# Kernel tuning notes

Measured on AMD Instinct MI355X. Metric: run time of the kernel, lower is better.

## Reference

```python
import jax, jax.numpy as jnp
import numpy as np

B, S, HID = 2, 2048, 2048
H, D = 16, 128  # heads, head_dim == kernel_hidden_size
GATE_NORM = 16.0
CLAMP_MIN = -50.0


def gla(q, k, v, gk):
    # fused_recurrent_gla: S_t = diag(exp(gk_t)) S_{t-1} + k_t^T v_t; o_t = (q_t*scale) @ S_t
    # q,k,v,gk: [B,H,S,D]
    scale = D ** -0.5
    qs = jnp.moveaxis(q, 2, 0) * scale  # [S,B,H,D]
    ks = jnp.moveaxis(k, 2, 0)
    vs = jnp.moveaxis(v, 2, 0)
    gs = jnp.moveaxis(gk, 2, 0)

    def step(state, xs):
        q_t, k_t, v_t, g_t = xs  # each [B,H,D]
        state = state * jnp.exp(g_t)[..., None] + k_t[..., None] * v_t[..., None, :]
        o_t = jnp.einsum('bhk,bhkv->bhv', q_t, state)
        return state, o_t

    init = jnp.zeros((q.shape[0], H, D, D), q.dtype)
    _, out = jax.lax.scan(step, init, (qs, ks, vs, gs))
    return jnp.moveaxis(out, 0, 2)  # [B,H,S,D]


def setup_inputs() -> dict:
    key = jax.random.key(0)
    ks = jax.random.split(key, 8)
    std = 0.02
    hidden_states = jax.random.normal(ks[0], (B, S, HID), jnp.float32)
    Wq = jax.random.normal(ks[1], (HID, HID), jnp.float32) * std
    Wk = jax.random.normal(ks[2], (HID, HID), jnp.float32) * std
    Wv = jax.random.normal(ks[3], (HID, HID), jnp.float32) * std
    Wo = jax.random.normal(ks[4], (HID, HID), jnp.float32) * std
    Wg1 = jnp.eye(HID, dtype=jnp.float32)  # nn.init.eye_
    bg1 = jnp.zeros((HID,), jnp.float32)
    Wg2 = jnp.eye(HID, dtype=jnp.float32)
    bg2 = jnp.zeros((HID,), jnp.float32)
    alpha_list = jax.random.uniform(ks[5], (2,), jnp.float32)
    return dict(hidden_states=hidden_states, Wq=Wq, Wk=Wk, Wv=Wv, Wo=Wo,
                Wg1=Wg1, bg1=bg1, Wg2=Wg2, bg2=bg2, alpha_list=alpha_list)


def reference(hidden_states, Wq, Wk, Wv, Wo, Wg1, bg1, Wg2, bg2, alpha_list):
    b, s, _ = hidden_states.shape

    def split_heads(x):  # [b,s,hid] -> [b,h,s,d]
        return x.reshape(b, s, H, D).transpose(0, 2, 1, 3)

    q = split_heads(hidden_states @ Wq.T)
    k = split_heads(hidden_states @ Wk.T)
    v = split_heads(hidden_states @ Wv.T)

    def gate(Wg, bg):
        g = split_heads(hidden_states @ Wg.T + bg)
        g = jax.nn.log_sigmoid(g) / GATE_NORM
        return jnp.maximum(g, CLAMP_MIN)

    gk = gate(Wg1, bg1)
    gk2 = gate(Wg2, bg2)

    o1 = gla(q, k, v, gk)
    o2 = gla(q, k, v, gk2)

    a = jax.nn.softmax(alpha_list)
    attn = a[0] * o1 + a[1] * o2  # [b,h,s,d]
    attn = attn.transpose(0, 2, 1, 3).reshape(b, s, HID)
    return attn @ Wo.T
```

## Files before the change

### kernel.cpp

```cpp
#include <hip/hip_runtime.h>
#include <cstdint>
#include <cstddef>


#define BB     2
#define SEQ    2048
#define HIDN   2048
#define NH     16
#define DD     128
#define CHUNK  64
#define NCHUNK (SEQ / CHUNK)
#define NBH    (BB * NH)
#define NELC   8388608
#define WELC   4194304
static constexpr float QSCALE = 0.08838834764831845f;

typedef __bf16 bf16_t;
typedef short  short8 __attribute__((ext_vector_type(8)));
typedef __bf16 bf16x8 __attribute__((ext_vector_type(8)));
typedef __bf16 bf16x4 __attribute__((ext_vector_type(4)));
typedef float  f32x4  __attribute__((ext_vector_type(4)));

__device__ __forceinline__ int swz16(int r, int c) {
  return r * 128 + ((((c >> 3) ^ r) & 15) << 3) + (c & 7);
}
__device__ __forceinline__ int swz16c(int r, int ch) {
  return r * 128 + (((ch ^ r) & 15) << 3);
}
__device__ __forceinline__ int swz8(int r, int c) {
  return r * 64 + ((((c >> 3) ^ r) & 7) << 3) + (c & 7);
}
__device__ __forceinline__ int swz8c(int r, int ch) {
  return r * 64 + (((ch ^ r) & 7) << 3);
}

__device__ __forceinline__ void gload_lds16(const void* g, void* l) {
  __builtin_amdgcn_global_load_lds(
      (__attribute__((address_space(1))) unsigned int*)g,
      (__attribute__((address_space(3))) unsigned int*)l, 16, 0, 0);
}

__device__ __forceinline__ void gemm_body(const bf16_t* __restrict__ A,
                                          const bf16_t* __restrict__ Bw,
                                          const float*  __restrict__ bias,
                                          bf16_t* __restrict__ outb,
                                          float*  __restrict__ outf, int epi) {
  __shared__ bf16_t As[128 * 32];
  __shared__ bf16_t Bs[128 * 32];
  const int tm   = blockIdx.x * 128;
  const int tn   = blockIdx.y * 128;
  const int wave = threadIdx.x >> 6;
  const int lane = threadIdx.x & 63;
  const int wm   = (wave >> 1) * 64;
  const int wn   = (wave & 1) * 64;
  const int qd   = lane >> 4;
  const int l16  = lane & 15;

  const int c0 = (wave * 2 + 0) * 64 + lane;
  const int c1 = (wave * 2 + 1) * 64 + lane;
  const bf16_t* ga0 = A  + (size_t)(tm + (c0 >> 2)) * HIDN + (c0 & 3) * 8;
  const bf16_t* ga1 = A  + (size_t)(tm + (c1 >> 2)) * HIDN + (c1 & 3) * 8;
  const bf16_t* gb0 = Bw + (size_t)(tn + (c0 >> 2)) * HIDN + (c0 & 3) * 8;
  const bf16_t* gb1 = Bw + (size_t)(tn + (c1 >> 2)) * HIDN + (c1 & 3) * 8;
  bf16_t* la0 = &As[(wave * 2 + 0) * 512];
  bf16_t* la1 = &As[(wave * 2 + 1) * 512];
  bf16_t* lb0 = &Bs[(wave * 2 + 0) * 512];
  bf16_t* lb1 = &Bs[(wave * 2 + 1) * 512];

  f32x4 acc[4][4];
#pragma unroll
  for (int i = 0; i < 4; i++)
#pragma unroll
    for (int j = 0; j < 4; j++) acc[i][j] = (f32x4){0.f, 0.f, 0.f, 0.f};

  for (int k0 = 0; k0 < HIDN; k0 += 32) {
    gload_lds16(ga0, la0); gload_lds16(ga1, la1);
    gload_lds16(gb0, lb0); gload_lds16(gb1, lb1);
    ga0 += 32; ga1 += 32; gb0 += 32; gb1 += 32;
    __syncthreads();
    short8 af[4], bfv[4];
#pragma unroll
    for (int t = 0; t < 4; t++)
      af[t] = *(const short8*)&As[(wm + t * 16 + l16) * 32 + qd * 8];
#pragma unroll
    for (int t = 0; t < 4; t++)
      bfv[t] = *(const short8*)&Bs[(wn + t * 16 + l16) * 32 + qd * 8];
#pragma unroll
    for (int i = 0; i < 4; i++)
#pragma unroll
      for (int j = 0; j < 4; j++)
        acc[i][j] = __builtin_amdgcn_mfma_f32_16x16x32_bf16(af[i], bfv[j],
                                                            acc[i][j], 0, 0, 0);
    __syncthreads();
  }

#pragma unroll
  for (int i = 0; i < 4; i++)
#pragma unroll
    for (int j = 0; j < 4; j++)
#pragma unroll
      for (int r = 0; r < 4; r++) {
        const int row = tm + wm + i * 16 + qd * 4 + r;
        const int col = tn + wn + j * 16 + l16;
        float v = acc[i][j][r];
        if (epi == 1) {
          v += bias[col];
          const float ls = fminf(v, 0.f) - log1pf(__expf(-fabsf(v)));
          v = fmaxf(ls * 0.0625f, -50.f);
        }
        if (epi == 2) outf[(size_t)row * HIDN + col] = v;
        else          outb[(size_t)row * HIDN + col] = (bf16_t)v;
      }
}

__global__ __launch_bounds__(256) void k_gemm_proj(
    const bf16_t* __restrict__ Xb,
    const bf16_t* __restrict__ W0, const bf16_t* __restrict__ W1,
    const bf16_t* __restrict__ W2, const bf16_t* __restrict__ W3,
    const bf16_t* __restrict__ W4,
    const float* __restrict__ bg1, const float* __restrict__ bg2,
    bf16_t* __restrict__ Qb, bf16_t* __restrict__ Kb, bf16_t* __restrict__ Vb,
    bf16_t* __restrict__ G1b, bf16_t* __restrict__ G2b) {
  const int z = blockIdx.z;
  const bf16_t* Ws[5] = {W0, W1, W2, W3, W4};
  bf16_t* Os[5] = {Qb, Kb, Vb, G1b, G2b};
  const float* bias = (z == 3) ? bg1 : ((z == 4) ? bg2 : nullptr);
  gemm_body(Xb, Ws[z], bias, Os[z], nullptr, (z >= 3) ? 1 : 0);
}

__global__ __launch_bounds__(256) void k_gemm_out(
    const bf16_t* __restrict__ attnB, const bf16_t* __restrict__ Wob,
    float* __restrict__ out) {
  gemm_body(attnB, Wob, nullptr, nullptr, out, 2);
}

__global__ __launch_bounds__(256) void k_cvt_all(
    const float* __restrict__ hid, const float* __restrict__ wq,
    const float* __restrict__ wk, const float* __restrict__ wv,
    const float* __restrict__ wg1, const float* __restrict__ wg2,
    bf16_t* __restrict__ Xb, bf16_t* __restrict__ Wout,
    bf16_t* __restrict__ Wcur) {
  const int y = blockIdx.y;
  const float* srcs[6] = {hid, wq, wk, wv, wg1, wg2};
  bf16_t* dsts[6] = {Xb, Wout, Wout + WELC, Wout + 2 * WELC, Wout + 3 * WELC,
                     Wcur};
  const int n = (y == 0) ? NELC : WELC;
  const float* src = srcs[y];
  bf16_t* dst = dsts[y];
  const int idx = (blockIdx.x * 256 + threadIdx.x) * 4;
  if (idx < n) {
    const float4 f = *(const float4*)(src + idx);
    bf16x4 o;
    o[0] = (bf16_t)f.x; o[1] = (bf16_t)f.y; o[2] = (bf16_t)f.z; o[3] = (bf16_t)f.w;
    *(bf16x4*)(dst + idx) = o;
  }
}

__global__ __launch_bounds__(256) void k_cvt(const float* __restrict__ src,
                                             bf16_t* __restrict__ dst, int n) {
  const int idx = (blockIdx.x * 256 + threadIdx.x) * 4;
  if (idx < n) {
    const float4 f = *(const float4*)(src + idx);
    bf16x4 o;
    o[0] = (bf16_t)f.x; o[1] = (bf16_t)f.y; o[2] = (bf16_t)f.z; o[3] = (bf16_t)f.w;
    *(bf16x4*)(dst + idx) = o;
  }
}

__global__ __launch_bounds__(256) void k_zero(float* __restrict__ out) {
  out[(size_t)blockIdx.x * 256 + threadIdx.x] = 0.f;
}

__global__ __launch_bounds__(256) void k_s1(
    const bf16_t* __restrict__ Kb, const bf16_t* __restrict__ Vb,
    const bf16_t* __restrict__ G, bf16_t* __restrict__ UT,
    float* __restrict__ Btot) {
  const int n = blockIdx.x, bh = blockIdx.y;
  const int b = bh >> 4, h = bh & 15;
  const int tid = threadIdx.x;
  __shared__ bf16_t vT[128 * 64];
  __shared__ bf16_t khT[128 * 64];
  const size_t base = ((size_t)(b * SEQ + n * CHUNK)) * HIDN + h * DD;

  if (tid < DD) {
    const int d = tid;
    float c = 0.f;
    for (int t = 0; t < CHUNK; t++) c += (float)G[base + (size_t)t * HIDN + d];
    const float Bt = c;
    Btot[((size_t)bh * NCHUNK + n) * DD + d] = Bt;
    c = 0.f;
    for (int t = 0; t < CHUNK; t++) {
      c += (float)G[base + (size_t)t * HIDN + d];
      khT[swz8(d, t)] =
          (bf16_t)((float)Kb[base + (size_t)t * HIDN + d] * __expf(Bt - c));
    }
  } else {
    const int t2 = tid - 128;
    for (int i = t2; i < CHUNK * DD; i += 128) {
      const int t = i >> 7, d = i & 127;
      vT[swz8(d, t)] = Vb[base + (size_t)t * HIDN + d];
    }
  }
  __syncthreads();

  const int wave = tid >> 6, lane = tid & 63, qd = lane >> 4, l16 = lane & 15;
  const int m0 = (wave >> 1) * 64;
  const int n0 = (wave & 1) * 64;
  f32x4 acc[4][4];
#pragma unroll
  for (int i = 0; i < 4; i++)
#pragma unroll
    for (int j = 0; j < 4; j++) acc[i][j] = (f32x4){0.f, 0.f, 0.f, 0.f};
#pragma unroll
  for (int ks = 0; ks < 2; ks++) {
    const int ch = ks * 4 + qd;
    short8 af[4], bfv[4];
#pragma unroll
    for (int i = 0; i < 4; i++)
      af[i] = *(const short8*)&vT[swz8c(m0 + i * 16 + l16, ch)];
#pragma unroll
    for (int j = 0; j < 4; j++)
      bfv[j] = *(const short8*)&khT[swz8c(n0 + j * 16 + l16, ch)];
#pragma unroll
    for (int i = 0; i < 4; i++)
#pragma unroll
      for (int j = 0; j < 4; j++)
        acc[i][j] = __builtin_amdgcn_mfma_f32_16x16x32_bf16(af[i], bfv[j],
                                                            acc[i][j], 0, 0, 0);
  }
  bf16_t* Uo = UT + ((size_t)bh * NCHUNK + n) * (size_t)(DD * DD);
#pragma unroll
  for (int i = 0; i < 4; i++)
#pragma unroll
    for (int j = 0; j < 4; j++)
#pragma unroll
      for (int r = 0; r < 4; r++)
        Uo[(size_t)(m0 + i * 16 + qd * 4 + r) * DD + n0 + j * 16 + l16] =
            (bf16_t)acc[i][j][r];
}

__global__ __launch_bounds__(256) void k_s2(bf16_t* __restrict__ UT,
                                            const float* __restrict__ Btot) {
  const int dg = blockIdx.x, bh = blockIdx.y;
  const int dv = dg * 8 + (threadIdx.x >> 5);
  const int dk0 = (threadIdx.x & 31) * 4;
  float st[4] = {0.f, 0.f, 0.f, 0.f};
  for (int nn = 0; nn < NCHUNK; nn++) {
    bf16_t* p =
        UT + ((size_t)bh * NCHUNK + nn) * (size_t)(DD * DD) + dv * DD + dk0;
    const float4 bp =
        *(const float4*)(Btot + ((size_t)bh * NCHUNK + nn) * DD + dk0);
    const bf16x4 u = *(const bf16x4*)p;
    bf16x4 sv;
#pragma unroll
    for (int j = 0; j < 4; j++) sv[j] = (bf16_t)st[j];
    *(bf16x4*)p = sv;
    st[0] = st[0] * __expf(bp.x) + (float)u[0];
    st[1] = st[1] * __expf(bp.y) + (float)u[1];
    st[2] = st[2] * __expf(bp.z) + (float)u[2];
    st[3] = st[3] * __expf(bp.w) + (float)u[3];
  }
}

template <int ACC>
__global__ __launch_bounds__(256) void k_s3(
    const bf16_t* __restrict__ Qb, const bf16_t* __restrict__ Kb,
    const bf16_t* __restrict__ Vb, const bf16_t* __restrict__ G,
    const bf16_t* __restrict__ UT, const float* __restrict__ alpha,
    bf16_t* __restrict__ attn) {
  const int n = blockIdx.x, bh = blockIdx.y;
  const int b = bh >> 4, h = bh & 15;
  const int tid = threadIdx.x;
  __shared__ bf16_t qh2[64 * 128];
  __shared__ bf16_t k2v[64 * 128];
  __shared__ bf16_t Ps[64 * 64];
  const size_t base = ((size_t)(b * SEQ + n * CHUNK)) * HIDN + h * DD;
  const float mx = fmaxf(alpha[0], alpha[1]);
  const float x0 = __expf(alpha[0] - mx), x1 = __expf(alpha[1] - mx);
  const float w = (ACC ? x1 : x0) / (x0 + x1);

  if (tid < DD) {
    const int d = tid;
    const float wsc = w * QSCALE;
    float c = 0.f;
    for (int t = 0; t < CHUNK; t++) {
      c += (float)G[base + (size_t)t * HIDN + d];
      const float ec = __expf(c);
      qh2[swz16(t, d)] =
          (bf16_t)((float)Qb[base + (size_t)t * HIDN + d] * wsc * ec);
      k2v[swz16(t, d)] =
          (bf16_t)((float)Kb[base + (size_t)t * HIDN + d] * __expf(-c));
    }
  }
  __syncthreads();

  const int wave = tid >> 6, lane = tid & 63, qd = lane >> 4, l16 = lane & 15;
  {
    f32x4 pacc[4];
#pragma unroll
    for (int j = 0; j < 4; j++) pacc[j] = (f32x4){0.f, 0.f, 0.f, 0.f};
#pragma unroll
    for (int ks = 0; ks < 4; ks++) {
      const int ch = ks * 4 + qd;
      const short8 a = *(const short8*)&qh2[swz16c(wave * 16 + l16, ch)];
#pragma unroll
      for (int j = 0; j < 4; j++) {
        const short8 bq = *(const short8*)&k2v[swz16c(j * 16 + l16, ch)];
        pacc[j] = __builtin_amdgcn_mfma_f32_16x16x32_bf16(a, bq, pacc[j], 0, 0, 0);
      }
    }
#pragma unroll
    for (int j = 0; j < 4; j++)
#pragma unroll
      for (int r = 0; r < 4; r++) {
        const int t = wave * 16 + qd * 4 + r, s = j * 16 + l16;
        Ps[swz8(t, s)] = (t >= s) ? (bf16_t)pacc[j][r] : (bf16_t)0.f;
      }
  }
  __syncthreads();
  for (int i = tid; i < CHUNK * DD; i += 256) {
    const int t = i >> 7, d = i & 127;
    k2v[swz8(d, t)] = Vb[base + (size_t)t * HIDN + d];
  }
  __syncthreads();

  const bf16_t* Sp = UT + ((size_t)bh * NCHUNK + n) * (size_t)(DD * DD);
  const int nw = wave * 32;
  f32x4 acc[4][2];
#pragma unroll
  for (int i = 0; i < 4; i++)
#pragma unroll
    for (int j = 0; j < 2; j++) acc[i][j] = (f32x4){0.f, 0.f, 0.f, 0.f};
#pragma unroll
  for (int ks = 0; ks < 2; ks++) {
    const int ch = ks * 4 + qd;
    short8 a[4];
#pragma unroll
    for (int i = 0; i < 4; i++)
      a[i] = *(const short8*)&Ps[swz8c(i * 16 + l16, ch)];
#pragma unroll
    for (int j = 0; j < 2; j++) {
      const short8 bq = *(const short8*)&k2v[swz8c(nw + j * 16 + l16, ch)];
#pragma unroll
      for (int i = 0; i < 4; i++)
        acc[i][j] = __builtin_amdgcn_mfma_f32_16x16x32_bf16(a[i], bq,
                                                            acc[i][j], 0, 0, 0);
    }
  }
#pragma unroll
  for (int ks = 0; ks < 4; ks++) {
    const int ch = ks * 4 + qd;
    short8 a[4];
#pragma unroll
    for (int i = 0; i < 4; i++)
      a[i] = *(const short8*)&qh2[swz16c(i * 16 + l16, ch)];
#pragma unroll
    for (int j = 0; j < 2; j++) {
      const short8 bq =
          *(const short8*)(Sp + (size_t)(nw + j * 16 + l16) * DD + ks * 32 + qd * 8);
#pragma unroll
      for (int i = 0; i < 4; i++)
        acc[i][j] = __builtin_amdgcn_mfma_f32_16x16x32_bf16(a[i], bq,
                                                            acc[i][j], 0, 0, 0);
    }
  }
#pragma unroll
  for (int i = 0; i < 4; i++)
#pragma unroll
    for (int j = 0; j < 2; j++)
#pragma unroll
      for (int r = 0; r < 4; r++) {
        const int t = i * 16 + qd * 4 + r;
        const int dv = nw + j * 16 + l16;
        bf16_t* p = &attn[base + (size_t)t * HIDN + dv];
        if (ACC) *p = (bf16_t)((float)*p + acc[i][j][r]);
        else     *p = (bf16_t)acc[i][j][r];
      }
}

extern "C" void kernel_launch(void* const* d_in, const int* in_sizes, int n_in,
                              void* d_out, int out_size, void* d_ws,
                              size_t ws_size, hipStream_t stream) {
  const float* hid  = (const float*)d_in[0];
  const float* wq   = (const float*)d_in[1];
  const float* wk   = (const float*)d_in[2];
  const float* wv   = (const float*)d_in[3];
  const float* wo   = (const float*)d_in[4];
  const float* wg1  = (const float*)d_in[5];
  const float* bg1  = (const float*)d_in[6];
  const float* wg2  = (const float*)d_in[7];
  const float* bg2  = (const float*)d_in[8];
  const float* alph = (const float*)d_in[9];
  float* out = (float*)d_out;
  (void)in_sizes; (void)n_in; (void)out_size;

  char* ws = (char*)d_ws;
  size_t off = 0;
  auto alloc = [&](size_t bytes) -> void* {
    void* p = ws + off;
    off += (bytes + 255) & ~(size_t)255;
    return p;
  };
  const size_t NEL = NELC, WEL = WELC;
  bf16_t* Xb   = (bf16_t*)alloc(NEL * 2);
  bf16_t* Wcur = (bf16_t*)alloc(WEL * 2);
  bf16_t* Qb   = (bf16_t*)alloc(NEL * 2);
  bf16_t* Kb   = (bf16_t*)alloc(NEL * 2);
  bf16_t* Vb   = (bf16_t*)alloc(NEL * 2);
  bf16_t* G1b  = (bf16_t*)alloc(NEL * 2);
  bf16_t* G2b  = (bf16_t*)alloc(NEL * 2);
  float*  Btot = (float*) alloc((size_t)NBH * NCHUNK * DD * 4);
  bf16_t* Wd = (bf16_t*)d_out;
  bf16_t* UT = (bf16_t*)d_out;

  if (off > ws_size) {
    k_zero<<<dim3((unsigned)(NEL / 256)), 256, 0, stream>>>(out);
    return;
  }

  k_cvt_all<<<dim3(8192, 6), 256, 0, stream>>>(hid, wq, wk, wv, wg1, wg2, Xb,
                                               Wd, Wcur);
  k_gemm_proj<<<dim3(32, 16, 5), 256, 0, stream>>>(
      Xb, Wd, Wd + WEL, Wd + 2 * WEL, Wd + 3 * WEL, Wcur, bg1, bg2, Qb, Kb, Vb,
      G1b, G2b);

  const dim3 gs(NCHUNK, NBH), g2(16, NBH);
  k_s1<<<gs, 256, 0, stream>>>(Kb, Vb, G1b, UT, Btot);
  k_s2<<<g2, 256, 0, stream>>>(UT, Btot);
  k_s3<0><<<gs, 256, 0, stream>>>(Qb, Kb, Vb, G1b, UT, alph, Xb);
  k_s1<<<gs, 256, 0, stream>>>(Kb, Vb, G2b, UT, Btot);
  k_s2<<<g2, 256, 0, stream>>>(UT, Btot);
  k_s3<1><<<gs, 256, 0, stream>>>(Qb, Kb, Vb, G2b, UT, alph, Xb);

  k_cvt<<<4096, 256, 0, stream>>>(wo, Wcur, (int)WEL);
  k_gemm_out<<<dim3(32, 16), 256, 0, stream>>>(Xb, Wcur, out);
}
```

Before: 617.9 us.

## Pre-transpose chunk tiles and cumsum gates, widen GEMM K-tile to 64

Adds a k_trg pass that rewrites each 64x128 chunk of Q/K/V/G in place into a d-major layout. For the gates it stores the prefix cumsum as fp16 and records per-chunk totals for both gates. The s1 and s3 kernels then read transposed rows with vector loads instead of doing strided per-element gathers and serial cumsums. V is now read directly from global memory rather than staged into LDS. The projection GEMM doubles its K tile to 64 with an XOR-swizzled LDS layout, and the Wo conversion is folded into the initial conversion kernel. This trades an extra full read/write pass over five activation buffers and fp16 storage of the cumsums for cheaper chunk kernels and fewer barriers.

Result: slower. 648.5 us (+4.9%).

```diff
diff --git a/kernel.cpp b/kernel.cpp
--- a/kernel.cpp
+++ b/kernel.cpp
@@ -16,22 +16,22 @@
 static constexpr float QSCALE = 0.08838834764831845f;
 
 typedef __bf16 bf16_t;
+typedef _Float16 half_t;
 typedef short  short8 __attribute__((ext_vector_type(8)));
-typedef __bf16 bf16x8 __attribute__((ext_vector_type(8)));
-typedef __bf16 bf16x4 __attribute__((ext_vector_type(4)));
 typedef float  f32x4  __attribute__((ext_vector_type(4)));
-
-__device__ __forceinline__ int swz16(int r, int c) {
-  return r * 128 + ((((c >> 3) ^ r) & 15) << 3) + (c & 7);
-}
-__device__ __forceinline__ int swz16c(int r, int ch) {
-  return r * 128 + (((ch ^ r) & 15) << 3);
-}
-__device__ __forceinline__ int swz8(int r, int c) {
-  return r * 64 + ((((c >> 3) ^ r) & 7) << 3) + (c & 7);
-}
-__device__ __forceinline__ int swz8c(int r, int ch) {
-  return r * 64 + (((ch ^ r) & 7) << 3);
+typedef float  float4v __attribute__((ext_vector_type(4)));
+
+__device__ __forceinline__ float bf2f(short u) {
+  return (float)__builtin_bit_cast(bf16_t, u);
+}
+__device__ __forceinline__ short f2bf(float f) {
+  return __builtin_bit_cast(short, (bf16_t)f);
+}
+__device__ __forceinline__ float hf2f(short u) {
+  return (float)__builtin_bit_cast(half_t, u);
+}
+__device__ __forceinline__ short f2hf(float f) {
+  return __builtin_bit_cast(short, (half_t)f);
 }
 
 __device__ __forceinline__ void gload_lds16(const void* g, void* l) {
@@ -45,8 +45,8 @@
                                           const float*  __restrict__ bias,
                                           bf16_t* __restrict__ outb,
                                           float*  __restrict__ outf, int epi) {
-  __shared__ bf16_t As[128 * 32];
-  __shared__ bf16_t Bs[128 * 32];
+  __shared__ bf16_t As[128 * 64];
+  __shared__ bf16_t Bs[128 * 64];
   const int tm   = blockIdx.x * 128;
   const int tn   = blockIdx.y * 128;
   const int wave = threadIdx.x >> 6;
@@ -55,17 +55,21 @@
   const int wn   = (wave & 1) * 64;
   const int qd   = lane >> 4;
   const int l16  = lane & 15;
-
-  const int c0 = (wave * 2 + 0) * 64 + lane;
-  const int c1 = (wave * 2 + 1) * 64 + lane;
-  const bf16_t* ga0 = A  + (size_t)(tm + (c0 >> 2)) * HIDN + (c0 & 3) * 8;
-  const bf16_t* ga1 = A  + (size_t)(tm + (c1 >> 2)) * HIDN + (c1 & 3) * 8;
-  const bf16_t* gb0 = Bw + (size_t)(tn + (c0 >> 2)) * HIDN + (c0 & 3) * 8;
-  const bf16_t* gb1 = Bw + (size_t)(tn + (c1 >> 2)) * HIDN + (c1 & 3) * 8;
-  bf16_t* la0 = &As[(wave * 2 + 0) * 512];
-  bf16_t* la1 = &As[(wave * 2 + 1) * 512];
-  bf16_t* lb0 = &Bs[(wave * 2 + 0) * 512];
-  bf16_t* lb1 = &Bs[(wave * 2 + 1) * 512];
+  const int ro   = l16 & 7;
+
+  const int gc   = (lane & 7) ^ (lane >> 3);
+  const bf16_t* ga[4];
+  const bf16_t* gb[4];
+  bf16_t* la[4];
+  bf16_t* lb[4];
+#pragma unroll
+  for (int u = 0; u < 4; u++) {
+    const int row = wave * 32 + u * 8 + (lane >> 3);
+    ga[u] = A  + (size_t)(tm + row) * HIDN + gc * 8;
+    gb[u] = Bw + (size_t)(tn + row) * HIDN + gc * 8;
+    la[u] = &As[(wave * 256 + u * 64) * 8];
+    lb[u] = &Bs[(wave * 256 + u * 64) * 8];
+  }
 
   f32x4 acc[4][4];
 #pragma unroll
@@ -73,24 +77,29 @@
 #pragma unroll
     for (int j = 0; j < 4; j++) acc[i][j] = (f32x4){0.f, 0.f, 0.f, 0.f};
 
-  for (int k0 = 0; k0 < HIDN; k0 += 32) {
-    gload_lds16(ga0, la0); gload_lds16(ga1, la1);
-    gload_lds16(gb0, lb0); gload_lds16(gb1, lb1);
-    ga0 += 32; ga1 += 32; gb0 += 32; gb1 += 32;
+  for (int k0 = 0; k0 < HIDN; k0 += 64) {
+#pragma unroll
+    for (int u = 0; u < 4; u++) { gload_lds16(ga[u], la[u]); ga[u] += 64; }
+#pragma unroll
+    for (int u = 0; u < 4; u++) { gload_lds16(gb[u], lb[u]); gb[u] += 64; }
     __syncthreads();
-    short8 af[4], bfv[4];
-#pragma unroll
-    for (int t = 0; t < 4; t++)
-      af[t] = *(const short8*)&As[(wm + t * 16 + l16) * 32 + qd * 8];
-#pragma unroll
-    for (int t = 0; t < 4; t++)
-      bfv[t] = *(const short8*)&Bs[(wn + t * 16 + l16) * 32 + qd * 8];
-#pragma unroll
-    for (int i = 0; i < 4; i++)
-#pragma unroll
-      for (int j = 0; j < 4; j++)
-        acc[i][j] = __builtin_amdgcn_mfma_f32_16x16x32_bf16(af[i], bfv[j],
-                                                            acc[i][j], 0, 0, 0);
+#pragma unroll
+    for (int ks = 0; ks < 2; ks++) {
+      const int g = ks * 4 + qd;
+      short8 af[4], bfv[4];
+#pragma unroll
+      for (int t = 0; t < 4; t++)
+        af[t] = *(const short8*)&As[(wm + t * 16 + l16) * 64 + (g ^ ro) * 8];
+#pragma unroll
+      for (int t = 0; t < 4; t++)
+        bfv[t] = *(const short8*)&Bs[(wn + t * 16 + l16) * 64 + (g ^ ro) * 8];
+#pragma unroll
+      for (int i = 0; i < 4; i++)
+#pragma unroll
+        for (int j = 0; j < 4; j++)
+          acc[i][j] = __builtin_amdgcn_mfma_f32_16x16x32_bf16(
+              af[i], bfv[j], acc[i][j], 0, 0, 0);
+    }
     __syncthreads();
   }
 
@@ -138,32 +147,21 @@
     const float* __restrict__ hid, const float* __restrict__ wq,
     const float* __restrict__ wk, const float* __restrict__ wv,
     const float* __restrict__ wg1, const float* __restrict__ wg2,
-    bf16_t* __restrict__ Xb, bf16_t* __restrict__ Wout,
-    bf16_t* __restrict__ Wcur) {
+    const float* __restrict__ wo, bf16_t* __restrict__ Xb,
+    bf16_t* __restrict__ Wd, bf16_t* __restrict__ Wcur,
+    bf16_t* __restrict__ WoB) {
   const int y = blockIdx.y;
-  const float* srcs[6] = {hid, wq, wk, wv, wg1, wg2};
-  bf16_t* dsts[6] = {Xb, Wout, Wout + WELC, Wout + 2 * WELC, Wout + 3 * WELC,
-                     Wcur};
+  const float* srcs[7] = {hid, wq, wk, wv, wg1, wg2, wo};
+  bf16_t* dsts[7] = {Xb, Wd, Wd + WELC, Wd + 2 * WELC, Wd + 3 * WELC, Wcur,
+                     WoB};
   const int n = (y == 0) ? NELC : WELC;
   const float* src = srcs[y];
   bf16_t* dst = dsts[y];
   const int idx = (blockIdx.x * 256 + threadIdx.x) * 4;
   if (idx < n) {
     const float4 f = *(const float4*)(src + idx);
-    bf16x4 o;
-    o[0] = (bf16_t)f.x; o[1] = (bf16_t)f.y; o[2] = (bf16_t)f.z; o[3] = (bf16_t)f.w;
-    *(bf16x4*)(dst + idx) = o;
-  }
-}
-
-__global__ __launch_bounds__(256) void k_cvt(const float* __restrict__ src,
-                                             bf16_t* __restrict__ dst, int n) {
-  const int idx = (blockIdx.x * 256 + threadIdx.x) * 4;
-  if (idx < n) {
-    const float4 f = *(const float4*)(src + idx);
-    bf16x4 o;
-    o[0] = (bf16_t)f.x; o[1] = (bf16_t)f.y; o[2] = (bf16_t)f.z; o[3] = (bf16_t)f.w;
-    *(bf16x4*)(dst + idx) = o;
+    dst[idx + 0] = (bf16_t)f.x; dst[idx + 1] = (bf16_t)f.y;
+    dst[idx + 2] = (bf16_t)f.z; dst[idx + 3] = (bf16_t)f.w;
   }
 }
 
@@ -171,41 +169,95 @@
   out[(size_t)blockIdx.x * 256 + threadIdx.x] = 0.f;
 }
 
+__global__ __launch_bounds__(256) void k_trg(
+    bf16_t* __restrict__ Qb, bf16_t* __restrict__ Kb, bf16_t* __restrict__ Vb,
+    bf16_t* __restrict__ G1b, bf16_t* __restrict__ G2b,
+    float* __restrict__ Btot) {
+  const int n = blockIdx.x, bh = blockIdx.y, z = blockIdx.z;
+  const int b = bh >> 4, h = bh & 15;
+  bf16_t* bufs[5] = {Qb, Kb, Vb, G1b, G2b};
+  short* P = (short*)bufs[z];
+  const size_t rbase = ((size_t)(b * SEQ + n * CHUNK)) * HIDN + h * DD;
+  const int tid = threadIdx.x;
+  __shared__ short L1[CHUNK * 136];
+  __shared__ short L2[DD * 72];
+
+#pragma unroll
+  for (int k = 0; k < 4; k++) {
+    const int v = tid + k * 256;
+    const int t = v >> 4, d0 = (v & 15) * 8;
+    const short8 x = *(const short8*)(P + rbase + (size_t)t * HIDN + d0);
+#pragma unroll
+    for (int j = 0; j < 8; j++) L1[t * 136 + d0 + j] = x[j];
+  }
+  __syncthreads();
+  if (tid < DD) {
+    const int d = tid;
+    if (z >= 3) {
+      float c = 0.f;
+#pragma unroll
+      for (int ch = 0; ch < 8; ch++) {
+        short8 o;
+#pragma unroll
+        for (int j = 0; j < 8; j++) {
+          c += bf2f(L1[(ch * 8 + j) * 136 + d]);
+          o[j] = f2hf(c);
+        }
+        *(short8*)&L2[d * 72 + ch * 8] = o;
+      }
+      Btot[((size_t)((z - 3) * NBH + bh) * NCHUNK + n) * DD + d] = c;
+    } else {
+#pragma unroll
+      for (int ch = 0; ch < 8; ch++) {
+        short8 o;
+#pragma unroll
+        for (int j = 0; j < 8; j++) o[j] = L1[(ch * 8 + j) * 136 + d];
+        *(short8*)&L2[d * 72 + ch * 8] = o;
+      }
+    }
+  }
+  __syncthreads();
+#pragma unroll
+  for (int k = 0; k < 4; k++) {
+    const int v = tid + k * 256;
+    const int r = v >> 4, x0 = (v & 15) * 8;
+    const int d = 2 * r + (x0 >> 6), t0 = x0 & 63;
+    const short8 o = *(const short8*)&L2[d * 72 + t0];
+    *(short8*)(P + rbase + (size_t)r * HIDN + x0) = o;
+  }
+}
+
 __global__ __launch_bounds__(256) void k_s1(
     const bf16_t* __restrict__ Kb, const bf16_t* __restrict__ Vb,
-    const bf16_t* __restrict__ G, bf16_t* __restrict__ UT,
-    float* __restrict__ Btot) {
+    const bf16_t* __restrict__ Gc, bf16_t* __restrict__ UT) {
   const int n = blockIdx.x, bh = blockIdx.y;
   const int b = bh >> 4, h = bh & 15;
+  const size_t rbase = ((size_t)(b * SEQ + n * CHUNK)) * HIDN + h * DD;
   const int tid = threadIdx.x;
-  __shared__ bf16_t vT[128 * 64];
-  __shared__ bf16_t khT[128 * 64];
-  const size_t base = ((size_t)(b * SEQ + n * CHUNK)) * HIDN + h * DD;
+  __shared__ short k2L[DD * 72];
 
   if (tid < DD) {
     const int d = tid;
-    float c = 0.f;
-    for (int t = 0; t < CHUNK; t++) c += (float)G[base + (size_t)t * HIDN + d];
-    const float Bt = c;
-    Btot[((size_t)bh * NCHUNK + n) * DD + d] = Bt;
-    c = 0.f;
-    for (int t = 0; t < CHUNK; t++) {
-      c += (float)G[base + (size_t)t * HIDN + d];
-      khT[swz8(d, t)] =
-          (bf16_t)((float)Kb[base + (size_t)t * HIDN + d] * __expf(Bt - c));
-    }
-  } else {
-    const int t2 = tid - 128;
-    for (int i = t2; i < CHUNK * DD; i += 128) {
-      const int t = i >> 7, d = i & 127;
-      vT[swz8(d, t)] = Vb[base + (size_t)t * HIDN + d];
+    const size_t row = rbase + (size_t)(d >> 1) * HIDN + (d & 1) * 64;
+    const short* Kp = (const short*)Kb + row;
+    const short* Gp = (const short*)Gc + row;
+    const float c63 = hf2f(Gp[63]);
+#pragma unroll
+    for (int ch = 0; ch < 8; ch++) {
+      const short8 kk = *(const short8*)(Kp + ch * 8);
+      const short8 cc = *(const short8*)(Gp + ch * 8);
+      short8 o;
+#pragma unroll
+      for (int j = 0; j < 8; j++)
+        o[j] = f2bf(bf2f(kk[j]) * __expf(c63 - hf2f(cc[j])));
+      *(short8*)&k2L[d * 72 + ch * 8] = o;
     }
   }
   __syncthreads();
 
   const int wave = tid >> 6, lane = tid & 63, qd = lane >> 4, l16 = lane & 15;
-  const int m0 = (wave >> 1) * 64;
-  const int n0 = (wave & 1) * 64;
+  const int m0 = (wave >> 1) * 64, n0 = (wave & 1) * 64;
+  const short* Vp = (const short*)Vb;
   f32x4 acc[4][4];
 #pragma unroll
   for (int i = 0; i < 4; i++)
@@ -216,11 +268,14 @@
     const int ch = ks * 4 + qd;
     short8 af[4], bfv[4];
 #pragma unroll
-    for (int i = 0; i < 4; i++)
-      af[i] = *(const short8*)&vT[swz8c(m0 + i * 16 + l16, ch)];
+    for (int i = 0; i < 4; i++) {
+      const int dv = m0 + i * 16 + l16;
+      af[i] = *(const short8*)(Vp + rbase + (size_t)(dv >> 1) * HIDN +
+                               (dv & 1) * 64 + ch * 8);
+    }
 #pragma unroll
     for (int j = 0; j < 4; j++)
-      bfv[j] = *(const short8*)&khT[swz8c(n0 + j * 16 + l16, ch)];
+      bfv[j] = *(const short8*)&k2L[(n0 + j * 16 + l16) * 72 + ch * 8];
 #pragma unroll
     for (int i = 0; i < 4; i++)
 #pragma unroll
@@ -246,50 +301,56 @@
   const int dk0 = (threadIdx.x & 31) * 4;
   float st[4] = {0.f, 0.f, 0.f, 0.f};
   for (int nn = 0; nn < NCHUNK; nn++) {
-    bf16_t* p =
-        UT + ((size_t)bh * NCHUNK + nn) * (size_t)(DD * DD) + dv * DD + dk0;
-    const float4 bp =
-        *(const float4*)(Btot + ((size_t)bh * NCHUNK + nn) * DD + dk0);
-    const bf16x4 u = *(const bf16x4*)p;
-    bf16x4 sv;
-#pragma unroll
-    for (int j = 0; j < 4; j++) sv[j] = (bf16_t)st[j];
-    *(bf16x4*)p = sv;
-    st[0] = st[0] * __expf(bp.x) + (float)u[0];
-    st[1] = st[1] * __expf(bp.y) + (float)u[1];
-    st[2] = st[2] * __expf(bp.z) + (float)u[2];
-    st[3] = st[3] * __expf(bp.w) + (float)u[3];
+    short* p =
+        (short*)UT + ((size_t)bh * NCHUNK + nn) * (size_t)(DD * DD) + dv * DD + dk0;
+    const float4v bp =
+        *(const float4v*)(Btot + ((size_t)bh * NCHUNK + nn) * DD + dk0);
+    short u0 = p[0], u1 = p[1], u2 = p[2], u3 = p[3];
+    p[0] = f2bf(st[0]); p[1] = f2bf(st[1]);
+    p[2] = f2bf(st[2]); p[3] = f2bf(st[3]);
+    st[0] = st[0] * __expf(bp[0]) + bf2f(u0);
+    st[1] = st[1] * __expf(bp[1]) + bf2f(u1);
+    st[2] = st[2] * __expf(bp[2]) + bf2f(u2);
+    st[3] = st[3] * __expf(bp[3]) + bf2f(u3);
   }
 }
 
 template <int ACC>
 __global__ __launch_bounds__(256) void k_s3(
     const bf16_t* __restrict__ Qb, const bf16_t* __restrict__ Kb,
-    const bf16_t* __restrict__ Vb, const bf16_t* __restrict__ G,
+    const bf16_t* __restrict__ Vb, const bf16_t* __restrict__ Gc,
     const bf16_t* __restrict__ UT, const float* __restrict__ alpha,
     bf16_t* __restrict__ attn) {
   const int n = blockIdx.x, bh = blockIdx.y;
   const int b = bh >> 4, h = bh & 15;
+  const size_t rbase = ((size_t)(b * SEQ + n * CHUNK)) * HIDN + h * DD;
   const int tid = threadIdx.x;
-  __shared__ bf16_t qh2[64 * 128];
-  __shared__ bf16_t k2v[64 * 128];
-  __shared__ bf16_t Ps[64 * 64];
-  const size_t base = ((size_t)(b * SEQ + n * CHUNK)) * HIDN + h * DD;
+  __shared__ short qhL[CHUNK * 136];
+  __shared__ short k2L[CHUNK * 136];
+  __shared__ short PsL[CHUNK * 72];
   const float mx = fmaxf(alpha[0], alpha[1]);
   const float x0 = __expf(alpha[0] - mx), x1 = __expf(alpha[1] - mx);
   const float w = (ACC ? x1 : x0) / (x0 + x1);
 
   if (tid < DD) {
     const int d = tid;
+    const size_t row = rbase + (size_t)(d >> 1) * HIDN + (d & 1) * 64;
+    const short* Qp = (const short*)Qb + row;
+    const short* Kp = (const short*)Kb + row;
+    const short* Gp = (const short*)Gc + row;
     const float wsc = w * QSCALE;
-    float c = 0.f;
-    for (int t = 0; t < CHUNK; t++) {
-      c += (float)G[base + (size_t)t * HIDN + d];
-      const float ec = __expf(c);
-      qh2[swz16(t, d)] =
-          (bf16_t)((float)Qb[base + (size_t)t * HIDN + d] * wsc * ec);
-      k2v[swz16(t, d)] =
-          (bf16_t)((float)Kb[base + (size_t)t * HIDN + d] * __expf(-c));
+#pragma unroll
+    for (int ch = 0; ch < 8; ch++) {
+      const short8 qq = *(const short8*)(Qp + ch * 8);
+      const short8 kk = *(const short8*)(Kp + ch * 8);
+      const short8 cc = *(const short8*)(Gp + ch * 8);
+#pragma unroll
+      for (int j = 0; j < 8; j++) {
+        const float c = hf2f(cc[j]);
+        const int t = ch * 8 + j;
+        qhL[t * 136 + d] = f2bf(bf2f(qq[j]) * wsc * __expf(c));
+        k2L[t * 136 + d] = f2bf(bf2f(kk[j]) * __expf(-c));
+      }
     }
   }
   __syncthreads();
@@ -302,10 +363,10 @@
 #pragma unroll
     for (int ks = 0; ks < 4; ks++) {
       const int ch = ks * 4 + qd;
-      const short8 a = *(const short8*)&qh2[swz16c(wave * 16 + l16, ch)];
+      const short8 a = *(const short8*)&qhL[(wave * 16 + l16) * 136 + ch * 8];
 #pragma unroll
       for (int j = 0; j < 4; j++) {
-        const short8 bq = *(const short8*)&k2v[swz16c(j * 16 + l16, ch)];
+        const short8 bq = *(const short8*)&k2L[(j * 16 + l16) * 136 + ch * 8];
         pacc[j] = __builtin_amdgcn_mfma_f32_16x16x32_bf16(a, bq, pacc[j], 0, 0, 0);
       }
     }
@@ -314,17 +375,14 @@
 #pragma unroll
       for (int r = 0; r < 4; r++) {
         const int t = wave * 16 + qd * 4 + r, s = j * 16 + l16;
-        Ps[swz8(t, s)] = (t >= s) ? (bf16_t)pacc[j][r] : (bf16_t)0.f;
+        PsL[t * 72 + s] = (t >= s) ? f2bf(pacc[j][r]) : (short)0;
       }
   }
   __syncthreads();
-  for (int i = tid; i < CHUNK * DD; i += 256) {
-    const int t = i >> 7, d = i & 127;
-    k2v[swz8(d, t)] = Vb[base + (size_t)t * HIDN + d];
-  }
-  __syncthreads();
-
-  const bf16_t* Sp = UT + ((size_t)bh * NCHUNK + n) * (size_t)(DD * DD);
+
+  const short* Sp =
+      (const short*)UT + ((size_t)bh * NCHUNK + n) * (size_t)(DD * DD);
+  const short* Vp = (const short*)Vb;
   const int nw = wave * 32;
   f32x4 acc[4][2];
 #pragma unroll
@@ -337,10 +395,12 @@
     short8 a[4];
 #pragma unroll
     for (int i = 0; i < 4; i++)
-      a[i] = *(const short8*)&Ps[swz8c(i * 16 + l16, ch)];
+      a[i] = *(const short8*)&PsL[(i * 16 + l16) * 72 + ch * 8];
 #pragma unroll
     for (int j = 0; j < 2; j++) {
-      const short8 bq = *(const short8*)&k2v[swz8c(nw + j * 16 + l16, ch)];
+      const int dv = nw + j * 16 + l16;
+      const short8 bq = *(const short8*)(Vp + rbase + (size_t)(dv >> 1) * HIDN +
+                                         (dv & 1) * 64 + ch * 8);
 #pragma unroll
       for (int i = 0; i < 4; i++)
         acc[i][j] = __builtin_amdgcn_mfma_f32_16x16x32_bf16(a[i], bq,
@@ -353,11 +413,11 @@
     short8 a[4];
 #pragma unroll
     for (int i = 0; i < 4; i++)
-      a[i] = *(const short8*)&qh2[swz16c(i * 16 + l16, ch)];
+      a[i] = *(const short8*)&qhL[(i * 16 + l16) * 136 + ch * 8];
 #pragma unroll
     for (int j = 0; j < 2; j++) {
       const short8 bq =
-          *(const short8*)(Sp + (size_t)(nw + j * 16 + l16) * DD + ks * 32 + qd * 8);
+          *(const short8*)(Sp + (size_t)(nw + j * 16 + l16) * DD + ch * 8);
 #pragma unroll
       for (int i = 0; i < 4; i++)
         acc[i][j] = __builtin_amdgcn_mfma_f32_16x16x32_bf16(a[i], bq,
@@ -372,7 +432,7 @@
       for (int r = 0; r < 4; r++) {
         const int t = i * 16 + qd * 4 + r;
         const int dv = nw + j * 16 + l16;
-        bf16_t* p = &attn[base + (size_t)t * HIDN + dv];
+        bf16_t* p = &attn[rbase + (size_t)t * HIDN + dv];
         if (ACC) *p = (bf16_t)((float)*p + acc[i][j][r]);
         else     *p = (bf16_t)acc[i][j][r];
       }
@@ -404,12 +464,13 @@
   const size_t NEL = NELC, WEL = WELC;
   bf16_t* Xb   = (bf16_t*)alloc(NEL * 2);
   bf16_t* Wcur = (bf16_t*)alloc(WEL * 2);
+  bf16_t* WoB  = (bf16_t*)alloc(WEL * 2);
   bf16_t* Qb   = (bf16_t*)alloc(NEL * 2);
   bf16_t* Kb   = (bf16_t*)alloc(NEL * 2);
   bf16_t* Vb   = (bf16_t*)alloc(NEL * 2);
   bf16_t* G1b  = (bf16_t*)alloc(NEL * 2);
   bf16_t* G2b  = (bf16_t*)alloc(NEL * 2);
-  float*  Btot = (float*) alloc((size_t)NBH * NCHUNK * DD * 4);
+  float*  Btot = (float*) alloc((size_t)2 * NBH * NCHUNK * DD * 4);
   bf16_t* Wd = (bf16_t*)d_out;
   bf16_t* UT = (bf16_t*)d_out;
 
@@ -418,20 +479,21 @@
     return;
   }
 
-  k_cvt_all<<<dim3(8192, 6), 256, 0, stream>>>(hid, wq, wk, wv, wg1, wg2, Xb,
-                                               Wd, Wcur);
+  k_cvt_all<<<dim3(8192, 7), 256, 0, stream>>>(hid, wq, wk, wv, wg1, wg2, wo,
+                                               Xb, Wd, Wcur, WoB);
   k_gemm_proj<<<dim3(32, 16, 5), 256, 0, stream>>>(
       Xb, Wd, Wd + WEL, Wd + 2 * WEL, Wd + 3 * WEL, Wcur, bg1, bg2, Qb, Kb, Vb,
       G1b, G2b);
+  k_trg<<<dim3(NCHUNK, NBH, 5), 256, 0, stream>>>(Qb, Kb, Vb, G1b, G2b, Btot);
 
   const dim3 gs(NCHUNK, NBH), g2(16, NBH);
-  k_s1<<<gs, 256, 0, stream>>>(Kb, Vb, G1b, UT, Btot);
+  const size_t BSTRIDE = (size_t)NBH * NCHUNK * DD;
+  k_s1<<<gs, 256, 0, stream>>>(Kb, Vb, G1b, UT);
   k_s2<<<g2, 256, 0, stream>>>(UT, Btot);
   k_s3<0><<<gs, 256, 0, stream>>>(Qb, Kb, Vb, G1b, UT, alph, Xb);
-  k_s1<<<gs, 256, 0, stream>>>(Kb, Vb, G2b, UT, Btot);
-  k_s2<<<g2, 256, 0, stream>>>(UT, Btot);
+  k_s1<<<gs, 256, 0, stream>>>(Kb, Vb, G2b, UT);
+  k_s2<<<g2, 256, 0, stream>>>(UT, Btot + BSTRIDE);
   k_s3<1><<<gs, 256, 0, stream>>>(Qb, Kb, Vb, G2b, UT, alph, Xb);
 
-  k_cvt<<<4096, 256, 0, stream>>>(wo, Wcur, (int)WEL);
-  k_gemm_out<<<dim3(32, 16), 256, 0, stream>>>(Xb, Wcur, out);
-}
+  k_gemm_out<<<dim3(32, 16), 256, 0, stream>>>(Xb, WoB, out);
+}
```
